# Kernel optimization log

Hardware: AMD Instinct MI355X
Metric: run time of the kernel (lower is better)

The kernel has to match this reference:

```python
import jax, jax.numpy as jnp
import numpy as np

N_NODES = 100000
N_EDGES = 1600000
D = 64
N_RELS = 200
LEAKY_SLOPE = 0.01


def setup_inputs() -> dict:
    key = jax.random.key(0)
    ks = jax.random.split(key, 12)
    def xavier(k, shape):
        gain = float(np.sqrt(2.0))  # calculate_gain('relu')
        bound = gain * float(np.sqrt(6.0 / (shape[0] + shape[1])))
        return jax.random.uniform(k, shape, jnp.float32, -bound, bound)
    return {
        "h": jax.random.normal(ks[0], (N_NODES, D), jnp.float32),
        "rel_emb": jax.random.normal(ks[1], (N_RELS, D), jnp.float32),
        "weight_neighbor": xavier(ks[2], (2 * D, D)),
        "attn_w": (xavier(ks[3], (3 * D, 1))).reshape(3 * D),
        "delta": jnp.ones((1,), jnp.float32),
        "loop_weight": xavier(ks[4], (D, D)),
        "evolve_loop_weight": xavier(ks[5], (D, D)),
        "etime": jax.random.uniform(ks[6], (N_EDGES,), jnp.float32),
        "src": jax.random.randint(ks[7], (N_EDGES,), 0, N_NODES),
        "dst": jax.random.randint(ks[8], (N_EDGES,), 0, N_NODES),
        "etype": jax.random.randint(ks[9], (N_EDGES,), 0, N_RELS),
    }


def reference(h, rel_emb, weight_neighbor, attn_w, delta, loop_weight,
              evolve_loop_weight, etime, src, dst, etype):
    N, d = h.shape
    # cat(src_h, rel) @ W  ==  src_h @ W[:d] + rel @ W[d:]  (precompute per node / per relation)
    hW = h @ weight_neighbor[:d]                 # [N, d]
    relW = rel_emb @ weight_neighbor[d:]         # [R, d]
    # attn_fc(cat(src_h, dst_h, rel)) == per-node/per-rel scalar contributions
    a1, a2, a3 = attn_w[:d], attn_w[d:2 * d], attn_w[2 * d:]
    s_src = h @ a1                               # [N]
    s_dst = h @ a2                               # [N]
    s_rel = rel_emb @ a3                         # [R]
    e = jax.nn.leaky_relu(s_src[src] + s_dst[dst] + s_rel[etype], LEAKY_SLOPE)  # [E]
    k = -etime * delta[0]                        # [E]
    scores = k * e                               # [E]
    # segment softmax over in-edges of each destination node
    m = jax.ops.segment_max(scores, dst, num_segments=N)          # [N]
    ex = jnp.exp(scores - m[dst])                                  # [E]
    den = jax.ops.segment_sum(ex, dst, num_segments=N)             # [N]
    w = ex / den[dst]                                              # [E]
    msg = hW[src] + relW[etype]                                    # [E, d]
    agg = jax.ops.segment_sum(w[:, None] * msg, dst, num_segments=N)  # [N, d]
    # nodes with no in-edges keep original h (DGL update_all semantics)
    deg = jax.ops.segment_sum(jnp.ones_like(scores), dst, num_segments=N)
    has_in = (deg > 0)[:, None]
    loop = jnp.where(has_in, h @ loop_weight, h @ evolve_loop_weight)
    node_repr = jnp.where(has_in, agg, h) + loop
    return node_repr
```

## Files before the change

### kernel.cpp

```cpp
#include <hip/hip_runtime.h>
#include <hip/hip_bf16.h>

#define N_NODES 100000
#define N_EDGES 1600000
#define D       64
#define N_RELS  200
#define LEAKY   0.01f
#define NBUCK   ((N_NODES + 511) / 512)
#define BIN_CHUNK 4096
#define NBIN    ((N_EDGES + BIN_CHUNK - 1) / BIN_CHUNK)

typedef __hip_bfloat16 bf16;

__device__ __forceinline__ float b2f(bf16 x) { return __bfloat162float(x); }
__device__ __forceinline__ bf16  f2b(float x) { return __float2bfloat16(x); }

__device__ __forceinline__ float ldf(const void* p, long i, int bf) {
    return bf ? __bfloat162float(((const bf16*)p)[i]) : ((const float*)p)[i];
}
__device__ __forceinline__ int probe_bf(const void* delta) {
    return ((const unsigned short*)delta)[0] == 0x3F80 ? 1 : 0;
}

__device__ __forceinline__ int rl_i(int v, int l) {
    return __builtin_amdgcn_readlane(v, l);
}
__device__ __forceinline__ float rl_f(float v, int l) {
    return __int_as_float(__builtin_amdgcn_readlane(__float_as_int(v), l));
}

__global__ __launch_bounds__(512, 4) void k_fused_proj(const void* __restrict__ h,
                                                       const void* __restrict__ wn,
                                                       const void* __restrict__ attn,
                                                       const void* __restrict__ delta,
                                                       const void* __restrict__ rel_emb,
                                                       const int* __restrict__ dst,
                                                       bf16* __restrict__ hWb,
                                                       float* __restrict__ s_src,
                                                       float* __restrict__ s_dst,
                                                       float* __restrict__ relW,
                                                       float* __restrict__ s_rel,
                                                       int* __restrict__ bcnt) {
    __shared__ int bh[NBUCK];
    const int bf = probe_bf(delta);
    const int wave = threadIdx.x >> 6;
    const int lane = threadIdx.x & 63;
    const int gw = blockIdx.x * 8 + wave;
    const int nwaves = gridDim.x * 8;
    float wreg[D];
    #pragma unroll
    for (int k = 0; k < D; k++) wreg[k] = ldf(wn, (long)k * D + lane, bf);
    const float a1 = ldf(attn, lane, bf);
    const float a2 = ldf(attn, D + lane, bf);
    for (int base = gw * 4; base < N_NODES; base += nwaves * 4) {
        float hv[4], acc[4];
        #pragma unroll
        for (int j = 0; j < 4; j++) {
            hv[j] = ldf(h, (long)(base + j) * D + lane, bf);
            acc[j] = 0.f;
        }
        #pragma unroll
        for (int j = 0; j < 4; j++) {
            float p1 = hv[j] * a1, p2 = hv[j] * a2;
            #pragma unroll
            for (int off = 32; off; off >>= 1) { p1 += __shfl_xor(p1, off); p2 += __shfl_xor(p2, off); }
            if (lane == 0) { s_src[base + j] = p1; s_dst[base + j] = p2; }
        }
        #pragma unroll
        for (int k = 0; k < D; k++) {
            float w = wreg[k];
            acc[0] += rl_f(hv[0], k) * w;
            acc[1] += rl_f(hv[1], k) * w;
            acc[2] += rl_f(hv[2], k) * w;
            acc[3] += rl_f(hv[3], k) * w;
        }
        #pragma unroll
        for (int j = 0; j < 4; j++) hWb[(long)(base + j) * D + lane] = f2b(acc[j]);
    }
    const float a3 = ldf(attn, 2 * D + lane, bf);
    for (int r = gw; r < N_RELS; r += nwaves) {
        float rv = ldf(rel_emb, (long)r * D + lane, bf);
        float p3 = rv * a3;
        #pragma unroll
        for (int off = 32; off; off >>= 1) p3 += __shfl_xor(p3, off);
        if (lane == 0) s_rel[r] = p3;
        float acc = 0.f;
        #pragma unroll
        for (int k = 0; k < D; k++) {
            acc += rl_f(rv, k) * ldf(wn, (long)(D + k) * D + lane, bf);
        }
        relW[r * D + lane] = acc;
    }
    for (int t = threadIdx.x; t < NBUCK; t += 512) bh[t] = 0;
    __syncthreads();
    for (int t = blockIdx.x * 512 + threadIdx.x; t < N_EDGES; t += gridDim.x * 512)
        atomicAdd(&bh[dst[t] >> 9], 1);
    __syncthreads();
    for (int t = threadIdx.x; t < NBUCK; t += 512) {
        int v = bh[t];
        if (v) atomicAdd(&bcnt[t], v);
    }
}

__global__ __launch_bounds__(256) void k_bscan(const int* __restrict__ bcnt,
                                               int* __restrict__ bbase,
                                               int* __restrict__ bcursor,
                                               int* __restrict__ rowptr) {
    __shared__ int s[256];
    const int tid = threadIdx.x;
    int v = (tid < NBUCK) ? bcnt[tid] : 0;
    s[tid] = v;
    __syncthreads();
    for (int off = 1; off < 256; off <<= 1) {
        int t = (tid >= off) ? s[tid - off] : 0;
        __syncthreads();
        s[tid] += t;
        __syncthreads();
    }
    if (tid < NBUCK) {
        int e = s[tid] - v;
        bbase[tid] = e;
        bcursor[tid] = e;
    }
    if (tid == 255) {
        bbase[NBUCK] = s[255];
        rowptr[N_NODES] = s[255];
    }
}

__global__ __launch_bounds__(512, 2) void k_bin(const float* __restrict__ s_src,
                                                const float* __restrict__ s_dst,
                                                const float* __restrict__ s_rel,
                                                const void* __restrict__ etime,
                                                const void* __restrict__ delta,
                                                const int* __restrict__ src,
                                                const int* __restrict__ dst,
                                                const int* __restrict__ etype,
                                                int* __restrict__ bcursor,
                                                int4* __restrict__ binned) {
    __shared__ int lh[NBUCK];
    __shared__ int lbase[NBUCK];
    __shared__ int gbase[NBUCK];
    __shared__ int sc[256];
    __shared__ int4 stage[BIN_CHUNK];
    const int bf = probe_bf(delta);
    const float df = ldf(delta, 0, bf);
    const int tid = threadIdx.x;
    const int base = blockIdx.x * BIN_CHUNK;
    for (int t = tid; t < NBUCK; t += 512) lh[t] = 0;
    __syncthreads();
    int4 rc[8];
    int rk[8], bk[8];
    #pragma unroll
    for (int j = 0; j < 8; j++) {
        int e = base + j * 512 + tid;
        bk[j] = -1;
        if (e < N_EDGES) {
            int s = src[e], d = dst[e], r = etype[e];
            float scv = s_src[s] + s_dst[d] + s_rel[r];
            float lre = scv > 0.f ? scv : LEAKY * scv;
            float score = (-ldf(etime, e, bf) * df) * lre;
            rc[j].x = __float_as_int(__expf(score));
            rc[j].y = s | (r << 17);
            rc[j].z = d & 511;
            rc[j].w = 0;
            int b = d >> 9;
            bk[j] = b;
            rk[j] = atomicAdd(&lh[b], 1);
        }
    }
    __syncthreads();
    if (tid < 256) sc[tid] = (tid < NBUCK) ? lh[tid] : 0;
    __syncthreads();
    for (int off = 1; off < 256; off <<= 1) {
        int t = 0;
        if (tid < 256 && tid >= off) t = sc[tid - off];
        __syncthreads();
        if (tid < 256) sc[tid] += t;
        __syncthreads();
    }
    if (tid < NBUCK) {
        lbase[tid] = sc[tid] - lh[tid];
        if (lh[tid] > 0) gbase[tid] = atomicAdd(&bcursor[tid], lh[tid]);
    }
    __syncthreads();
    #pragma unroll
    for (int j = 0; j < 8; j++) {
        if (bk[j] >= 0) stage[lbase[bk[j]] + rk[j]] = rc[j];
    }
    __syncthreads();
    const int wave = tid >> 6, lane = tid & 63;
    for (int b = wave; b < NBUCK; b += 8) {
        int n = lh[b];
        if (!n) continue;
        int ls = lbase[b];
        int gd = gbase[b];
        for (int k = lane; k < n; k += 64) binned[gd + k] = stage[ls + k];
    }
}

__global__ __launch_bounds__(1024) void k_bucket(const int4* __restrict__ binned,
                                                 const int* __restrict__ bbase,
                                                 int* __restrict__ rowptr,
                                                 int2* __restrict__ sorted) {
    __shared__ int fh[512];
    __shared__ int fc[512];
    __shared__ int sc[512];
    const int tid = threadIdx.x;
    const int b = blockIdx.x;
    const int n0 = b << 9;
    const int s0 = bbase[b], s1 = bbase[b + 1];
    if (tid < 512) { fh[tid] = 0; fc[tid] = 0; }
    __syncthreads();
    for (int i = s0 + tid; i < s1; i += 1024) atomicAdd(&fh[binned[i].z], 1);
    __syncthreads();
    if (tid < 512) sc[tid] = fh[tid];
    __syncthreads();
    for (int off = 1; off < 512; off <<= 1) {
        int t = 0;
        if (tid < 512 && tid >= off) t = sc[tid - off];
        __syncthreads();
        if (tid < 512) sc[tid] += t;
        __syncthreads();
    }
    int excl = 0;
    if (tid < 512) excl = sc[tid] - fh[tid];
    __syncthreads();
    if (tid < 512) {
        fh[tid] = excl;
        if (n0 + tid < N_NODES) rowptr[n0 + tid] = s0 + excl;
    }
    __syncthreads();
    for (int i = s0 + tid; i < s1; i += 1024) {
        int4 r = binned[i];
        int p = s0 + fh[r.z] + atomicAdd(&fc[r.z], 1);
        sorted[p] = make_int2(r.x, r.y);
    }
}

__global__ __launch_bounds__(512, 6) void k_aggregate(const int* __restrict__ rowptr,
                                                      const int2* __restrict__ sorted,
                                                      const bf16* __restrict__ hWb,
                                                      const float* __restrict__ relW,
                                                      const void* __restrict__ h,
                                                      const void* __restrict__ loopW,
                                                      const void* __restrict__ evolveW,
                                                      const void* __restrict__ delta,
                                                      float* __restrict__ out) {
    const int bf = probe_bf(delta);
    __shared__ float WL[D * D];
    __shared__ float WE[D * D];
    for (int t = threadIdx.x; t < D * D; t += 512) { WL[t] = ldf(loopW, t, bf); WE[t] = ldf(evolveW, t, bf); }
    __syncthreads();
    const int wave = threadIdx.x >> 6;
    const int lane = threadIdx.x & 63;
    const int wstride = gridDim.x * 8;
    for (int i = blockIdx.x * 8 + wave; i < N_NODES; i += wstride) {
        int s0 = rowptr[i], e1 = rowptr[i + 1];
        float hv = ldf(h, (long)i * D + lane, bf);
        float acc;
        const float* W;
        if (e1 > s0) {
            float ls = 0.f;
            acc = 0.f;
            for (int c = s0; c < e1; c += 64) {
                int n = e1 - c; n = n > 64 ? 64 : n;
                float exl = 0.f; int pk = 0;
                if (lane < n) {
                    int2 rec = sorted[c + lane];
                    exl = __int_as_float(rec.x);
                    pk = rec.y;
                }
                float cs = exl;
                #pragma unroll
                for (int off = 32; off; off >>= 1) cs += __shfl_xor(cs, off);
                ls += cs;
                int j = 0;
                for (; j + 4 <= n; j += 4) {
                    float w0 = rl_f(exl, j),     w1 = rl_f(exl, j + 1);
                    float w2 = rl_f(exl, j + 2), w3 = rl_f(exl, j + 3);
                    int   p0 = rl_i(pk, j),      p1 = rl_i(pk, j + 1);
                    int   p2 = rl_i(pk, j + 2),  p3 = rl_i(pk, j + 3);
                    float m0 = b2f(hWb[(long)(p0 & 0x1FFFF) * D + lane]) + relW[(p0 >> 17) * D + lane];
                    float m1 = b2f(hWb[(long)(p1 & 0x1FFFF) * D + lane]) + relW[(p1 >> 17) * D + lane];
                    float m2 = b2f(hWb[(long)(p2 & 0x1FFFF) * D + lane]) + relW[(p2 >> 17) * D + lane];
                    float m3 = b2f(hWb[(long)(p3 & 0x1FFFF) * D + lane]) + relW[(p3 >> 17) * D + lane];
                    acc += w0 * m0;
                    acc += w1 * m1;
                    acc += w2 * m2;
                    acc += w3 * m3;
                }
                for (; j < n; j++) {
                    float w = rl_f(exl, j);
                    int   p = rl_i(pk, j);
                    acc += w * (b2f(hWb[(long)(p & 0x1FFFF) * D + lane]) + relW[(p >> 17) * D + lane]);
                }
            }
            acc *= 1.f / ls;
            W = WL;
        } else {
            acc = hv;
            W = WE;
        }
        #pragma unroll
        for (int k = 0; k < D; k++) {
            acc += rl_f(hv, k) * W[k * D + lane];
        }
        out[(long)i * D + lane] = acc;
    }
}

__global__ __launch_bounds__(256) void k_fallback(float* __restrict__ out) {
    int t = blockIdx.x * blockDim.x + threadIdx.x;
    if (t < N_NODES * D) out[t] = 0.f;
}

extern "C" void kernel_launch(void* const* d_in, const int* in_sizes, int n_in,
                              void* d_out, int out_size, void* d_ws, size_t ws_size,
                              hipStream_t stream) {
    const void* h       = d_in[0];
    const void* rel_emb = d_in[1];
    const void* wn      = d_in[2];
    const void* attn    = d_in[3];
    const void* delta   = d_in[4];
    const void* loopW   = d_in[5];
    const void* evolveW = d_in[6];
    const void* etime   = d_in[7];
    const int*  src     = (const int*)d_in[8];
    const int*  dst     = (const int*)d_in[9];
    const int*  etype   = (const int*)d_in[10];
    float* out = (float*)d_out;

    char* ws = (char*)d_ws;
    size_t off = 0;
    auto alloc = [&](size_t bytes) -> void* {
        off = (off + 255) & ~(size_t)255;
        void* p = ws + off;
        off += bytes;
        return p;
    };
    int4*  binned  = (int4*) alloc((size_t)N_EDGES * 16);
    int2*  sorted  = (int2*) alloc((size_t)N_EDGES * 8);
    bf16*  hWb     = (bf16*) alloc((size_t)N_NODES * D * 2);
    float* relW    = (float*)alloc((size_t)N_RELS * D * 4);
    float* s_src   = (float*)alloc((size_t)N_NODES * 4);
    float* s_dst   = (float*)alloc((size_t)N_NODES * 4);
    float* s_rel   = (float*)alloc((size_t)N_RELS * 4);
    int*   rowptr  = (int*)  alloc((size_t)(N_NODES + 1) * 4);
    int*   bcnt    = (int*)  alloc((size_t)NBUCK * 4);
    int*   bbase   = (int*)  alloc((size_t)(NBUCK + 1) * 4);
    int*   bcursor = (int*)  alloc((size_t)NBUCK * 4);

    if (ws_size < off) {
        k_fallback<<<(N_NODES * D + 255) / 256, 256, 0, stream>>>(out);
        return;
    }

    hipMemsetAsync(bcnt, 0, (size_t)NBUCK * 4, stream);
    k_fused_proj<<<1024, 512, 0, stream>>>(h, wn, attn, delta, rel_emb, dst,
                                           hWb, s_src, s_dst, relW, s_rel, bcnt);
    k_bscan<<<1, 256, 0, stream>>>(bcnt, bbase, bcursor, rowptr);
    k_bin<<<NBIN, 512, 0, stream>>>(s_src, s_dst, s_rel, etime, delta,
                                    src, dst, etype, bcursor, binned);
    k_bucket<<<NBUCK, 1024, 0, stream>>>(binned, bbase, rowptr, sorted);
    k_aggregate<<<4096, 512, 0, stream>>>(rowptr, sorted, hWb, relW, h, loopW, evolveW, delta, out);
}
```

Before: 309.8 us.

## Split self-loop matmul into separate kernel and vectorize edge gather per lane

Moves the per-node loop/evolve matmul into its own kernel that keeps loop weights in registers and processes four nodes per wave, writing the result into the reused binned buffer. The aggregate kernel now has each 16-lane group handle a different edge, with each lane loading 4 features via 8-byte bf16 and 16-byte relW vector loads, then reducing across groups. This cuts per-edge shuffle and scalar load overhead and frees LDS. In exchange it adds an extra kernel launch and an extra global write/read of the loop result.

```diff
diff --git a/kernel.cpp b/kernel.cpp
--- a/kernel.cpp
+++ b/kernel.cpp
@@ -238,31 +238,71 @@
     }
 }
 
-__global__ __launch_bounds__(512, 6) void k_aggregate(const int* __restrict__ rowptr,
+__global__ __launch_bounds__(512, 4) void k_loop(const void* __restrict__ h,
+                                                 const void* __restrict__ loopW,
+                                                 const void* __restrict__ evolveW,
+                                                 const void* __restrict__ delta,
+                                                 const int* __restrict__ rowptr,
+                                                 float* __restrict__ L) {
+    const int bf = probe_bf(delta);
+    const int wave = threadIdx.x >> 6;
+    const int lane = threadIdx.x & 63;
+    const int gw = blockIdx.x * 8 + wave;
+    const int nwaves = gridDim.x * 8;
+    float wreg[D];
+    #pragma unroll
+    for (int k = 0; k < D; k++) wreg[k] = ldf(loopW, (long)k * D + lane, bf);
+    for (int base = gw * 4; base < N_NODES; base += nwaves * 4) {
+        float hv[4], acc[4];
+        #pragma unroll
+        for (int j = 0; j < 4; j++) {
+            hv[j] = ldf(h, (long)(base + j) * D + lane, bf);
+            acc[j] = 0.f;
+        }
+        #pragma unroll
+        for (int k = 0; k < D; k++) {
+            float w = wreg[k];
+            acc[0] += rl_f(hv[0], k) * w;
+            acc[1] += rl_f(hv[1], k) * w;
+            acc[2] += rl_f(hv[2], k) * w;
+            acc[3] += rl_f(hv[3], k) * w;
+        }
+        int rp[5];
+        #pragma unroll
+        for (int j = 0; j < 5; j++) rp[j] = rowptr[base + j];
+        #pragma unroll
+        for (int j = 0; j < 4; j++) {
+            if (rp[j + 1] == rp[j]) {
+                float a = 0.f;
+                for (int k = 0; k < D; k++) a += rl_f(hv[j], k) * ldf(evolveW, (long)k * D + lane, bf);
+                acc[j] = a;
+            }
+            L[(long)(base + j) * D + lane] = acc[j];
+        }
+    }
+}
+
+__global__ __launch_bounds__(512, 8) void k_aggregate(const int* __restrict__ rowptr,
                                                       const int2* __restrict__ sorted,
                                                       const bf16* __restrict__ hWb,
                                                       const float* __restrict__ relW,
                                                       const void* __restrict__ h,
-                                                      const void* __restrict__ loopW,
-                                                      const void* __restrict__ evolveW,
+                                                      const float* __restrict__ L,
                                                       const void* __restrict__ delta,
                                                       float* __restrict__ out) {
     const int bf = probe_bf(delta);
-    __shared__ float WL[D * D];
-    __shared__ float WE[D * D];
-    for (int t = threadIdx.x; t < D * D; t += 512) { WL[t] = ldf(loopW, t, bf); WE[t] = ldf(evolveW, t, bf); }
-    __syncthreads();
     const int wave = threadIdx.x >> 6;
     const int lane = threadIdx.x & 63;
+    const int grp  = lane >> 4;
+    const int sub  = lane & 15;
+    const unsigned sub8  = (unsigned)sub << 3;
+    const unsigned sub16 = (unsigned)sub << 4;
     const int wstride = gridDim.x * 8;
     for (int i = blockIdx.x * 8 + wave; i < N_NODES; i += wstride) {
-        int s0 = rowptr[i], e1 = rowptr[i + 1];
-        float hv = ldf(h, (long)i * D + lane, bf);
-        float acc;
-        const float* W;
+        const int s0 = rowptr[i], e1 = rowptr[i + 1];
         if (e1 > s0) {
+            float ax = 0.f, ay = 0.f, az = 0.f, aw = 0.f;
             float ls = 0.f;
-            acc = 0.f;
             for (int c = s0; c < e1; c += 64) {
                 int n = e1 - c; n = n > 64 ? 64 : n;
                 float exl = 0.f; int pk = 0;
@@ -275,38 +315,49 @@
                 #pragma unroll
                 for (int off = 32; off; off >>= 1) cs += __shfl_xor(cs, off);
                 ls += cs;
-                int j = 0;
-                for (; j + 4 <= n; j += 4) {
-                    float w0 = rl_f(exl, j),     w1 = rl_f(exl, j + 1);
-                    float w2 = rl_f(exl, j + 2), w3 = rl_f(exl, j + 3);
-                    int   p0 = rl_i(pk, j),      p1 = rl_i(pk, j + 1);
-                    int   p2 = rl_i(pk, j + 2),  p3 = rl_i(pk, j + 3);
-                    float m0 = b2f(hWb[(long)(p0 & 0x1FFFF) * D + lane]) + relW[(p0 >> 17) * D + lane];
-                    float m1 = b2f(hWb[(long)(p1 & 0x1FFFF) * D + lane]) + relW[(p1 >> 17) * D + lane];
-                    float m2 = b2f(hWb[(long)(p2 & 0x1FFFF) * D + lane]) + relW[(p2 >> 17) * D + lane];
-                    float m3 = b2f(hWb[(long)(p3 & 0x1FFFF) * D + lane]) + relW[(p3 >> 17) * D + lane];
-                    acc += w0 * m0;
-                    acc += w1 * m1;
-                    acc += w2 * m2;
-                    acc += w3 * m3;
-                }
-                for (; j < n; j++) {
-                    float w = rl_f(exl, j);
-                    int   p = rl_i(pk, j);
-                    acc += w * (b2f(hWb[(long)(p & 0x1FFFF) * D + lane]) + relW[(p >> 17) * D + lane]);
+                #pragma unroll 2
+                for (int j = 0; j < n; j += 4) {
+                    float w = __shfl(exl, j + grp);
+                    int   p = __shfl(pk,  j + grp);
+                    unsigned hoff = ((unsigned)(p & 0x1FFFF) << 7) + sub8;
+                    unsigned roff = ((unsigned)(p >> 17) << 8) + sub16;
+                    uint2  hw = *(const uint2*) ((const char*)hWb  + hoff);
+                    float4 rw = *(const float4*)((const char*)relW + roff);
+                    float f0 = __uint_as_float(hw.x << 16);
+                    float f1 = __uint_as_float(hw.x & 0xFFFF0000u);
+                    float f2 = __uint_as_float(hw.y << 16);
+                    float f3 = __uint_as_float(hw.y & 0xFFFF0000u);
+                    ax += w * (f0 + rw.x);
+                    ay += w * (f1 + rw.y);
+                    az += w * (f2 + rw.z);
+                    aw += w * (f3 + rw.w);
                 }
             }
-            acc *= 1.f / ls;
-            W = WL;
+            ax += __shfl_xor(ax, 16); ax += __shfl_xor(ax, 32);
+            ay += __shfl_xor(ay, 16); ay += __shfl_xor(ay, 32);
+            az += __shfl_xor(az, 16); az += __shfl_xor(az, 32);
+            aw += __shfl_xor(aw, 16); aw += __shfl_xor(aw, 32);
+            if (grp == 0) {
+                const float inv = 1.f / ls;
+                const float4 l4 = *(const float4*)(L + (long)i * D + sub * 4);
+                float4 r;
+                r.x = ax * inv + l4.x;
+                r.y = ay * inv + l4.y;
+                r.z = az * inv + l4.z;
+                r.w = aw * inv + l4.w;
+                *(float4*)(out + (long)i * D + sub * 4) = r;
+            }
         } else {
-            acc = hv;
-            W = WE;
-        }
-        #pragma unroll
-        for (int k = 0; k < D; k++) {
-            acc += rl_f(hv, k) * W[k * D + lane];
-        }
-        out[(long)i * D + lane] = acc;
+            if (grp == 0) {
+                const float4 l4 = *(const float4*)(L + (long)i * D + sub * 4);
+                float4 r;
+                r.x = ldf(h, (long)i * D + sub * 4 + 0, bf) + l4.x;
+                r.y = ldf(h, (long)i * D + sub * 4 + 1, bf) + l4.y;
+                r.z = ldf(h, (long)i * D + sub * 4 + 2, bf) + l4.z;
+                r.w = ldf(h, (long)i * D + sub * 4 + 3, bf) + l4.w;
+                *(float4*)(out + (long)i * D + sub * 4) = r;
+            }
+        }
     }
 }
 
@@ -351,6 +402,8 @@
     int*   bbase   = (int*)  alloc((size_t)(NBUCK + 1) * 4);
     int*   bcursor = (int*)  alloc((size_t)NBUCK * 4);
 
+    float* L = (float*)binned;
+
     if (ws_size < off) {
         k_fallback<<<(N_NODES * D + 255) / 256, 256, 0, stream>>>(out);
         return;
@@ -363,5 +416,6 @@
     k_bin<<<NBIN, 512, 0, stream>>>(s_src, s_dst, s_rel, etime, delta,
                                     src, dst, etype, bcursor, binned);
     k_bucket<<<NBUCK, 1024, 0, stream>>>(binned, bbase, rowptr, sorted);
-    k_aggregate<<<4096, 512, 0, stream>>>(rowptr, sorted, hWb, relW, h, loopW, evolveW, delta, out);
-}
+    k_loop<<<1024, 512, 0, stream>>>(h, loopW, evolveW, delta, rowptr, L);
+    k_aggregate<<<2048, 512, 0, stream>>>(rowptr, sorted, hWb, relW, h, L, delta, out);
+}
```

Measured after the change: 578.2 us. 1.87x slower.
